# Kernel tuning notes

Measured on AMD Instinct MI355X. Metric: run time of the kernel, lower is better.

The kernel has to match this reference:

```python
import jax, jax.numpy as jnp
import numpy as np

N_NODES = 50000
N_EDGES = 1200000
N_REL = 40
N_BASES = 30
EMB = 64
HID = 128
N_GRAPHS = 64


def rgcn_layer(h, src, dst, edge_type, comp, basis, root, bias):
    # W_r = sum_b comp[r,b] * basis[b]  -> [R, in, out]
    W = jnp.einsum('rb,bio->rio', comp, basis)
    n = h.shape[0]
    # aggregate source features per (target node, relation): mean aggregation (PyG RGCNConv default)
    seg = dst * N_REL + edge_type                      # [E]
    msgs = h[src]                                      # [E, in]  (gather)
    agg = jax.ops.segment_sum(msgs, seg, num_segments=n * N_REL)
    agg = agg.reshape(n, N_REL, -1)                    # [N, R, in]
    cnt = jax.ops.segment_sum(jnp.ones((src.shape[0],), h.dtype), seg,
                              num_segments=n * N_REL).reshape(n, N_REL, 1)
    agg = agg / jnp.maximum(cnt, 1.0)
    out = jnp.einsum('nri,rio->no', agg, W) + h @ root + bias
    return out


def setup_inputs() -> dict:
    key = jax.random.key(0)
    ks = jax.random.split(key, 12)
    x = jnp.arange(N_NODES, dtype=jnp.int64) if jax.config.jax_enable_x64 else jnp.arange(N_NODES, dtype=jnp.int32)
    edge_index = jax.random.randint(ks[0], (2, N_EDGES), 0, N_NODES)
    edge_type = jax.random.randint(ks[1], (N_EDGES,), 0, N_REL)
    batch = jnp.sort(jax.random.randint(ks[2], (N_NODES,), 0, N_GRAPHS))
    s = 0.05
    node_emb = jax.random.normal(ks[3], (N_NODES, EMB), jnp.float32)
    comp1 = jax.random.normal(ks[4], (N_REL, N_BASES), jnp.float32) * s
    basis1 = jax.random.normal(ks[5], (N_BASES, EMB, HID), jnp.float32) * s
    root1 = jax.random.normal(ks[6], (EMB, HID), jnp.float32) * s
    bias1 = jnp.zeros((HID,), jnp.float32)
    comp2 = jax.random.normal(ks[7], (N_REL, N_BASES), jnp.float32) * s
    basis2 = jax.random.normal(ks[8], (N_BASES, HID, HID), jnp.float32) * s
    root2 = jax.random.normal(ks[9], (HID, HID), jnp.float32) * s
    bias2 = jnp.zeros((HID,), jnp.float32)
    return {"x": x, "edge_index": edge_index, "edge_type": edge_type, "batch": batch,
            "node_emb": node_emb,
            "comp1": comp1, "basis1": basis1, "root1": root1, "bias1": bias1,
            "comp2": comp2, "basis2": basis2, "root2": root2, "bias2": bias2}


def reference(x, edge_index, edge_type, batch, node_emb,
              comp1, basis1, root1, bias1, comp2, basis2, root2, bias2):
    src, dst = edge_index[0], edge_index[1]
    h = node_emb[x]                                              # embedding lookup
    h = jax.nn.relu(rgcn_layer(h, src, dst, edge_type, comp1, basis1, root1, bias1))
    h = jax.nn.relu(rgcn_layer(h, src, dst, edge_type, comp2, basis2, root2, bias2))
    # global mean pool over graphs in batch
    sums = jax.ops.segment_sum(h, batch, num_segments=N_GRAPHS)  # [G, HID]
    cnts = jax.ops.segment_sum(jnp.ones((h.shape[0],), h.dtype), batch,
                               num_segments=N_GRAPHS)[:, None]
    return sums / jnp.maximum(cnts, 1.0)
```

## Files before the change

### kernel.cpp

```cpp
#include <hip/hip_runtime.h>


#define N_NODES 50000
#define N_EDGES 1200000
#define N_REL   40
#define N_BASES 30
#define EMB     64
#define HID     128
#define N_GRAPHS 64

#define NKEYC_MAX 160
#define PERM_CAP  ((size_t)N_EDGES + (size_t)NKEYC_MAX * 256)
#define SP_EPB    1024

typedef float f32x4  __attribute__((ext_vector_type(4)));
typedef short bf16x8 __attribute__((ext_vector_type(8)));

__device__ __forceinline__ unsigned short f2bf(float x) {
    unsigned int u = __float_as_uint(x);
    u = (u + 0x7FFFu + ((u >> 16) & 1u)) >> 16;
    return (unsigned short)u;
}
__device__ __forceinline__ float bflo(unsigned int u) { return __uint_as_float(u << 16); }
__device__ __forceinline__ float bfhi(unsigned int u) { return __uint_as_float(u & 0xffff0000u); }

#define OFF_WF1   ((size_t)0)
#define OFF_WF2   ((size_t)163840)
#define OFF_CNT   ((size_t)491520)
#define OFF_H1    ((size_t)2491520)
#define OFF_H2    ((size_t)8891520)
#define OFF_HB1   ((size_t)15291520)
#define OFF_HB2   ((size_t)16891520)
#define OFF_CNTG  ((size_t)20091520)
#define OFF_POOL  ((size_t)20091584)
#define OFF_PSRC  ((size_t)20099776)
#define OFF_POS   ((size_t)21340736)
#define OFF_PDST  ((size_t)22581696)
#define OFF_HCR   ((size_t)23822656)
#define OFF_CCR   ((size_t)23822816)
#define OFF_POCR  ((size_t)23822976)
#define OFF_HD    ((size_t)23823168)
#define OFF_CD    ((size_t)23873168)
#define OFF_POD   ((size_t)23923168)
#define OFF_RF1   ((size_t)23973184)
#define OFF_RF2   ((size_t)23977280)
#define OFF_PM    ((size_t)23985472)

template <int IN, int KT>
__global__ void k_Wfrag(const float* __restrict__ comp, const float* __restrict__ basis,
                        unsigned short* __restrict__ Wf) {
    const int FR = IN * HID;
    int idx = blockIdx.x * blockDim.x + threadIdx.x;
    if (idx >= N_REL * FR) return;
    int r = idx / FR, F = idx - r * FR;
    int j = F & 7, lane = (F >> 3) & 63, tt = F >> 9;
    int kt = tt % KT, ct = tt / KT;
    int k = kt * 32 + (lane >> 4) * 8 + j;
    int c = ct * 16 + (lane & 15);
    float s = 0.f;
#pragma unroll
    for (int b = 0; b < N_BASES; ++b)
        s += comp[r * N_BASES + b] * basis[((size_t)b * IN + k) * HID + c];
    Wf[idx] = f2bf(s);
}

template <int IN, int KT>
__global__ void k_rootfrag(const float* __restrict__ root, unsigned short* __restrict__ rf) {
    int idx = blockIdx.x * blockDim.x + threadIdx.x;
    if (idx >= IN * HID) return;
    int j = idx & 7, lane = (idx >> 3) & 63, tt = idx >> 9;
    int kt = tt % KT, ct = tt / KT;
    int k = kt * 32 + (lane >> 4) * 8 + j;
    int c = ct * 16 + (lane & 15);
    rf[idx] = f2bf(root[k * HID + c]);
}

__global__ void k_count(const int* __restrict__ dst, const int* __restrict__ etype,
                        float* __restrict__ cnt_t) {
    int e = blockIdx.x * blockDim.x + threadIdx.x;
    if (e >= N_EDGES) return;
    atomicAdd(&cnt_t[(size_t)etype[e] * N_NODES + dst[e]], 1.0f);
}

__global__ void k_deg_inv(float* __restrict__ cnt_t, int* __restrict__ hist) {
    int n = blockIdx.x * blockDim.x + threadIdx.x;
    if (n >= N_NODES) return;
    float s = 0.f;
#pragma unroll 8
    for (int r = 0; r < N_REL; ++r) {
        float c = cnt_t[(size_t)r * N_NODES + n];
        s += c;
        cnt_t[(size_t)r * N_NODES + n] = 1.0f / fmaxf(c, 1.0f);
    }
    hist[n] = (int)(s + 0.5f);
}

__global__ void k_scan_d(const int* __restrict__ hist, int* __restrict__ po) {
    __shared__ int csum[256];
    int t = threadIdx.x;
    const int CH = (N_NODES + 255) / 256;
    int k0 = t * CH, k1 = min(k0 + CH, N_NODES);
    int s = 0;
    for (int k = k0; k < k1; ++k) s += hist[k];
    csum[t] = s;
    __syncthreads();
    if (t == 0) {
        int acc = 0;
        for (int i = 0; i < 256; ++i) { int v = csum[i]; csum[i] = acc; acc += v; }
        po[N_NODES] = acc;
    }
    __syncthreads();
    int base = csum[t];
    for (int k = k0; k < k1; ++k) { po[k] = base; base += hist[k]; }
}

__global__ void k_hist_cr(const int* __restrict__ dst, const int* __restrict__ etype,
                          int* __restrict__ hist, int chn, int nkeyc) {
    __shared__ int lh[NKEYC_MAX];
    int t = threadIdx.x;
    if (t < nkeyc) lh[t] = 0;
    __syncthreads();
    int e = blockIdx.x * blockDim.x + t;
    if (e < N_EDGES) atomicAdd(&lh[(dst[e] / chn) * N_REL + etype[e]], 1);
    __syncthreads();
    if (t < nkeyc && lh[t]) atomicAdd(&hist[t], lh[t]);
}

__global__ void k_scan_cr(const int* __restrict__ hist, int* __restrict__ po, int nkeyc) {
    if (threadIdx.x == 0) {
        int acc = 0;
        for (int k = 0; k < nkeyc; ++k) {
            po[k] = acc;
            acc += ((hist[k] + 255) >> 8) << 8;
        }
        po[nkeyc] = acc;
    }
}

__global__ void k_fill(int* __restrict__ ps_src, int* __restrict__ ps_os,
                       int* __restrict__ ps_dst, int dumprow) {
    for (size_t s = (size_t)blockIdx.x * blockDim.x + threadIdx.x; s < PERM_CAP;
         s += (size_t)gridDim.x * blockDim.x) {
        ps_src[s] = 0;
        ps_os[s] = dumprow;
        ps_dst[s] = 0;
    }
}

__global__ void k_scatter_s(const int* __restrict__ src, const int* __restrict__ dst,
                            const int* __restrict__ etype,
                            const int* __restrict__ po_cr, int* __restrict__ cur_cr,
                            const int* __restrict__ po_d, int* __restrict__ cur_d,
                            int* __restrict__ ps_src, int* __restrict__ ps_os,
                            int* __restrict__ ps_dst, int chn, int nkeyc) {
    __shared__ int lh[NKEYC_MAX], sbase[NKEYC_MAX];
    int t = threadIdx.x;
    if (t < nkeyc) lh[t] = 0;
    __syncthreads();
    int e0 = blockIdx.x * SP_EPB;
    int e_[4], key_[4];
#pragma unroll
    for (int i = 0; i < 4; ++i) {
        int e = e0 + t + i * 256;
        e_[i] = e;
        if (e < N_EDGES) {
            key_[i] = (dst[e] / chn) * N_REL + etype[e];
            atomicAdd(&lh[key_[i]], 1);
        }
    }
    __syncthreads();
    if (t < nkeyc) { if (lh[t]) sbase[t] = atomicAdd(&cur_cr[t], lh[t]); lh[t] = 0; }
    __syncthreads();
#pragma unroll
    for (int i = 0; i < 4; ++i) {
        if (e_[i] < N_EDGES) {
            int e = e_[i], key = key_[i];
            int d = dst[e];
            int p = atomicAdd(&lh[key], 1);
            int slot = po_cr[key] + sbase[key] + p;
            int os_g = po_d[d] + atomicAdd(&cur_d[d], 1);
            int os_l = os_g - po_d[(d / chn) * chn];
            ps_src[slot] = src[e];
            ps_os[slot] = os_l;
            ps_dst[slot] = d;
        }
    }
}

template <int IN, int KT>
__global__ __launch_bounds__(256, 4)
void k_rootgemm(const unsigned short* __restrict__ hb_in,
                const unsigned short* __restrict__ rf,
                const float* __restrict__ bias, float* __restrict__ h) {
    __shared__ unsigned short Wl[8 * KT * 64 * 8];
    {
        const f32x4* Wg = (const f32x4*)rf;
        f32x4* Wd = (f32x4*)Wl;
        for (int kk = threadIdx.x; kk < 8 * KT * 64; kk += 256) Wd[kk] = Wg[kk];
    }
    __syncthreads();

    int l = threadIdx.x & 63, wv = threadIdx.x >> 6;
    int lrow = l & 15, lk = l >> 4;
    int nbase = blockIdx.x * 64 + wv * 16;

    int nrow = min(nbase + lrow, N_NODES - 1);
    bf16x8 a[KT];
    const unsigned short* hrow = hb_in + (size_t)nrow * IN + lk * 8;
#pragma unroll
    for (int kt = 0; kt < KT; ++kt)
        a[kt] = *(const bf16x8*)(hrow + kt * 32);

    f32x4 acc[8];
#pragma unroll
    for (int ct = 0; ct < 8; ++ct) acc[ct] = (f32x4){0.f, 0.f, 0.f, 0.f};
#pragma unroll
    for (int ct = 0; ct < 8; ++ct) {
#pragma unroll
        for (int kt = 0; kt < KT; ++kt) {
            bf16x8 bb = *(const bf16x8*)(Wl + ((ct * KT + kt) * 64 + l) * 8);
            acc[ct] = __builtin_amdgcn_mfma_f32_16x16x32_bf16(a[kt], bb, acc[ct], 0, 0, 0);
        }
    }
#pragma unroll
    for (int q = 0; q < 4; ++q) {
        int n = nbase + lk * 4 + q;
        if (n < N_NODES) {
#pragma unroll
            for (int ct = 0; ct < 8; ++ct)
                h[(size_t)n * HID + ct * 16 + lrow] = acc[ct][q] + bias[ct * 16 + lrow];
        }
    }
}

template <int IN, int KT>
__global__ __launch_bounds__(256, 4)
void k_msg(const unsigned short* __restrict__ hb_in, const int* __restrict__ ps_src,
           const int* __restrict__ ps_os, const int* __restrict__ ps_dst,
           const float* __restrict__ invc_t,
           const int* __restrict__ po_cr,
           const unsigned short* __restrict__ Wf, unsigned int* __restrict__ pm) {
    __shared__ unsigned short Wl[8 * KT * 64 * 8];
    int slot0 = po_cr[0] + blockIdx.x * 256;
    if (slot0 >= po_cr[N_REL]) return;
    int r = 0;
    while (po_cr[r + 1] <= slot0) ++r;

    {
        const f32x4* Wg = (const f32x4*)(Wf + (size_t)r * (8 * KT * 64 * 8));
        f32x4* Wd = (f32x4*)Wl;
        for (int kk = threadIdx.x; kk < 8 * KT * 64; kk += 256) Wd[kk] = Wg[kk];
    }
    __syncthreads();

    int l = threadIdx.x & 63, wv = threadIdx.x >> 6;
    int lrow = l & 15, lk = l >> 4;
    const float* invr = invc_t + (size_t)r * N_NODES;

    for (int t = wv; t < 16; t += 4) {
        int slot = slot0 + t * 16 + lrow;
        int sv = ps_src[slot];
        int os = ps_os[slot];
        int d  = ps_dst[slot];
        float inv = invr[d];

        bf16x8 a[KT];
        const unsigned short* hrow = hb_in + (size_t)sv * IN + lk * 8;
#pragma unroll
        for (int kt = 0; kt < KT; ++kt)
            a[kt] = *(const bf16x8*)(hrow + kt * 32);

        f32x4 acc[8];
#pragma unroll
        for (int ct = 0; ct < 8; ++ct) acc[ct] = (f32x4){0.f, 0.f, 0.f, 0.f};
#pragma unroll
        for (int ct = 0; ct < 8; ++ct) {
#pragma unroll
            for (int kt = 0; kt < KT; ++kt) {
                bf16x8 bb = *(const bf16x8*)(Wl + ((ct * KT + kt) * 64 + l) * 8);
                acc[ct] = __builtin_amdgcn_mfma_f32_16x16x32_bf16(a[kt], bb, acc[ct], 0, 0, 0);
            }
        }
#pragma unroll
        for (int q = 0; q < 4; ++q) {
            int row = lk * 4 + q;
            int osq   = __shfl(os, row);
            float ivq = __shfl(inv, row);
            unsigned int* dp = pm + (size_t)osq * 64 + lrow;
#pragma unroll
            for (int cp = 0; cp < 4; ++cp) {
                unsigned int u = (unsigned int)f2bf(acc[2 * cp][q] * ivq)
                               | ((unsigned int)f2bf(acc[2 * cp + 1][q] * ivq) << 16);
                __builtin_nontemporal_store(u, dp + cp * 16);
            }
        }
    }
}

template <bool WRITE_HB>
__global__ __launch_bounds__(256, 8)
void k_reduce(const unsigned int* __restrict__ pm, const int* __restrict__ po_d,
              int n0chunk, int chn, float* __restrict__ h,
              unsigned short* __restrict__ hb_out) {
    int wv = threadIdx.x >> 6, p = threadIdx.x & 63;
    int n = n0chunk + blockIdx.x * 4 + wv;
    if (n >= n0chunk + chn) return;
    int pmbase = po_d[n0chunk];
    int b0 = po_d[n] - pmbase;
    int cn = po_d[n + 1] - pmbase - b0;
    float lo = 0.f, hi = 0.f;
    const unsigned int* rp = pm + (size_t)b0 * 64 + p;
    int k = 0;
    for (; k + 4 <= cn; k += 4) {
        unsigned int u0 = __builtin_nontemporal_load(rp);
        unsigned int u1 = __builtin_nontemporal_load(rp + 64);
        unsigned int u2 = __builtin_nontemporal_load(rp + 128);
        unsigned int u3 = __builtin_nontemporal_load(rp + 192);
        rp += 256;
        lo += bflo(u0) + bflo(u1) + bflo(u2) + bflo(u3);
        hi += bfhi(u0) + bfhi(u1) + bfhi(u2) + bfhi(u3);
    }
    for (; k < cn; ++k) {
        unsigned int u = __builtin_nontemporal_load(rp);
        rp += 64;
        lo += bflo(u); hi += bfhi(u);
    }
    int cA = (p & 15) + 32 * (p >> 4);
    float* hp = h + (size_t)n * HID;
    float vA = fmaxf(hp[cA] + lo, 0.f);
    float vB = fmaxf(hp[cA + 16] + hi, 0.f);
    hp[cA] = vA;
    hp[cA + 16] = vB;
    if (WRITE_HB) {
        hb_out[(size_t)n * HID + cA] = f2bf(vA);
        hb_out[(size_t)n * HID + cA + 16] = f2bf(vB);
    }
}

__global__ void k_cvt_emb(const float* __restrict__ emb, const int* __restrict__ x,
                          unsigned short* __restrict__ hb) {
    int idx = blockIdx.x * blockDim.x + threadIdx.x;
    if (idx >= N_NODES * (EMB / 4)) return;
    int n = idx / (EMB / 4), c4 = idx % (EMB / 4);
    int row = x[n];
    float4 v = *(const float4*)(emb + (size_t)row * EMB + c4 * 4);
    ushort4 o = {f2bf(v.x), f2bf(v.y), f2bf(v.z), f2bf(v.w)};
    *(ushort4*)(hb + (size_t)n * EMB + c4 * 4) = o;
}

__global__ void k_gcount2(const int* __restrict__ batch, float* __restrict__ cntG) {
    int g = threadIdx.x;
    if (g >= N_GRAPHS) return;
    int lo = 0, hi = N_NODES;
    while (lo < hi) { int m = (lo + hi) >> 1; if (batch[m] < g) lo = m + 1; else hi = m; }
    int lb0 = lo;
    lo = 0; hi = N_NODES;
    while (lo < hi) { int m = (lo + hi) >> 1; if (batch[m] < g + 1) lo = m + 1; else hi = m; }
    cntG[g] = (float)(lo - lb0);
}

__global__ void k_pool(const float* __restrict__ h, const int* __restrict__ batch,
                       float* __restrict__ acc) {
    const int CH = 64;
    int n0 = blockIdx.x * CH;
    int o = threadIdx.x;
    int nend = min(n0 + CH, N_NODES);
    if (n0 >= N_NODES) return;
    int curg = batch[n0];
    float run = 0.f;
    for (int n = n0; n < nend; ++n) {
        int g = batch[n];
        if (g != curg) {
            atomicAdd(&acc[(size_t)curg * HID + o], run);
            run = 0.f;
            curg = g;
        }
        run += h[(size_t)n * HID + o];
    }
    atomicAdd(&acc[(size_t)curg * HID + o], run);
}

__global__ void k_final(const float* __restrict__ acc, const float* __restrict__ cntG,
                        float* __restrict__ out) {
    int idx = blockIdx.x * blockDim.x + threadIdx.x;
    if (idx >= N_GRAPHS * HID) return;
    int g = idx >> 7;
    out[idx] = acc[idx] / fmaxf(cntG[g], 1.0f);
}

extern "C" void kernel_launch(void* const* d_in, const int* in_sizes, int n_in,
                              void* d_out, int out_size, void* d_ws, size_t ws_size,
                              hipStream_t stream) {
    const int*   x         = (const int*)d_in[0];
    const int*   edge_index= (const int*)d_in[1];
    const int*   etype     = (const int*)d_in[2];
    const int*   batch     = (const int*)d_in[3];
    const float* node_emb  = (const float*)d_in[4];
    const float* comp1     = (const float*)d_in[5];
    const float* basis1    = (const float*)d_in[6];
    const float* root1     = (const float*)d_in[7];
    const float* bias1     = (const float*)d_in[8];
    const float* comp2     = (const float*)d_in[9];
    const float* basis2    = (const float*)d_in[10];
    const float* root2     = (const float*)d_in[11];
    const float* bias2     = (const float*)d_in[12];
    float* out = (float*)d_out;

    const int* src = edge_index;
    const int* dst = edge_index + N_EDGES;

    float* ws = (float*)d_ws;
    unsigned short* Wf1 = (unsigned short*)(ws + OFF_WF1);
    unsigned short* Wf2 = (unsigned short*)(ws + OFF_WF2);
    float* cnt_t = ws + OFF_CNT;
    float* h1   = ws + OFF_H1;
    float* h2   = ws + OFF_H2;
    unsigned short* hb1 = (unsigned short*)(ws + OFF_HB1);
    unsigned short* hb2 = (unsigned short*)(ws + OFF_HB2);
    float* cntG = ws + OFF_CNTG;
    float* pool = ws + OFF_POOL;
    int*   ps_src = (int*)(ws + OFF_PSRC);
    int*   ps_os  = (int*)(ws + OFF_POS);
    int*   ps_dst = (int*)(ws + OFF_PDST);
    int*   hist_cr = (int*)(ws + OFF_HCR);
    int*   cur_cr  = (int*)(ws + OFF_CCR);
    int*   po_cr   = (int*)(ws + OFF_POCR);
    int*   hist_d  = (int*)(ws + OFF_HD);
    int*   cur_d   = (int*)(ws + OFF_CD);
    int*   po_d    = (int*)(ws + OFF_POD);
    unsigned short* rf1 = (unsigned short*)(ws + OFF_RF1);
    unsigned short* rf2 = (unsigned short*)(ws + OFF_RF2);
    unsigned int* pm = (unsigned int*)(ws + OFF_PM);

    size_t ws_floats = ws_size / sizeof(float);
    int nch = 4;
    if (ws_floats >= OFF_PM + ((size_t)N_EDGES / 1 + 12504) * 64) nch = 1;
    else if (ws_floats >= OFF_PM + ((size_t)N_EDGES / 2 + 12504) * 64) nch = 2;
    int chn = N_NODES / nch;
    int nkeyc = nch * N_REL;
    int capr = N_EDGES / nch + 12504;
    int gridm = (capr + 255) / 256 + N_REL;

    hipMemsetAsync(cnt_t, 0, (size_t)N_NODES * N_REL * sizeof(float), stream);
    hipMemsetAsync(cntG, 0, (size_t)(N_GRAPHS + N_GRAPHS * HID) * sizeof(float), stream);
    hipMemsetAsync(hist_cr, 0, 2 * NKEYC_MAX * sizeof(int), stream);
    hipMemsetAsync(cur_d, 0, N_NODES * sizeof(int), stream);

    k_count<<<(N_EDGES + 255) / 256, 256, 0, stream>>>(dst, etype, cnt_t);
    k_deg_inv<<<(N_NODES + 255) / 256, 256, 0, stream>>>(cnt_t, hist_d);
    k_scan_d<<<1, 256, 0, stream>>>(hist_d, po_d);
    k_hist_cr<<<(N_EDGES + 255) / 256, 256, 0, stream>>>(dst, etype, hist_cr, chn, nkeyc);
    k_scan_cr<<<1, 64, 0, stream>>>(hist_cr, po_cr, nkeyc);
    k_fill<<<2048, 256, 0, stream>>>(ps_src, ps_os, ps_dst, capr - 1);
    k_scatter_s<<<(N_EDGES + SP_EPB - 1) / SP_EPB, 256, 0, stream>>>(
        src, dst, etype, po_cr, cur_cr, po_d, cur_d, ps_src, ps_os, ps_dst, chn, nkeyc);

    k_Wfrag<EMB, 2><<<(N_REL * EMB * HID + 255) / 256, 256, 0, stream>>>(comp1, basis1, Wf1);
    k_Wfrag<HID, 4><<<(N_REL * HID * HID + 255) / 256, 256, 0, stream>>>(comp2, basis2, Wf2);
    k_rootfrag<EMB, 2><<<(EMB * HID + 255) / 256, 256, 0, stream>>>(root1, rf1);
    k_rootfrag<HID, 4><<<(HID * HID + 255) / 256, 256, 0, stream>>>(root2, rf2);

    k_cvt_emb<<<(N_NODES * (EMB / 4) + 255) / 256, 256, 0, stream>>>(node_emb, x, hb1);
    k_rootgemm<EMB, 2><<<(N_NODES + 63) / 64, 256, 0, stream>>>(hb1, rf1, bias1, h1);
    for (int c = 0; c < nch; ++c) {
        k_msg<EMB, 2><<<gridm, 256, 0, stream>>>(hb1, ps_src, ps_os, ps_dst, cnt_t,
                                                 po_cr + c * N_REL, Wf1, pm);
        k_reduce<true><<<chn / 4, 256, 0, stream>>>(pm, po_d, c * chn, chn, h1, hb2);
    }

    k_rootgemm<HID, 4><<<(N_NODES + 63) / 64, 256, 0, stream>>>(hb2, rf2, bias2, h2);
    for (int c = 0; c < nch; ++c) {
        k_msg<HID, 4><<<gridm, 256, 0, stream>>>(hb2, ps_src, ps_os, ps_dst, cnt_t,
                                                 po_cr + c * N_REL, Wf2, pm);
        k_reduce<false><<<chn / 4, 256, 0, stream>>>(pm, po_d, c * chn, chn, h2, nullptr);
    }

    k_gcount2<<<1, 64, 0, stream>>>(batch, cntG);
    k_pool<<<(N_NODES + 63) / 64, HID, 0, stream>>>(h2, batch, pool);
    k_final<<<(N_GRAPHS * HID + 255) / 256, 256, 0, stream>>>(pool, cntG, out);
}
```

Measured before the change: 1.021 ms.

## Fuse count and chunk histogram, fill only pad slots, precompute block relation table

Merges the per-edge count atomics and the chunk/relation histogram into one pass over the edge list, removing a kernel launch and a reread of dst/etype. The full-buffer fill of the permutation arrays is replaced by a per-key kernel that writes only the padding slots at the end of each bucket. A byte table mapping each 256-slot block to its relation is built once, so k_msg looks up its relation directly instead of walking the prefix array. This adds two small launches and relies on the scatter covering every non-pad slot.

```diff
diff --git a/kernel.cpp b/kernel.cpp
--- a/kernel.cpp
+++ b/kernel.cpp
@@ -44,7 +44,8 @@
 #define OFF_POD   ((size_t)23923168)
 #define OFF_RF1   ((size_t)23973184)
 #define OFF_RF2   ((size_t)23977280)
-#define OFF_PM    ((size_t)23985472)
+#define OFF_BREL  ((size_t)23985472)
+#define OFF_PM    ((size_t)23987520)
 
 template <int IN, int KT>
 __global__ void k_Wfrag(const float* __restrict__ comp, const float* __restrict__ basis,
@@ -75,11 +76,21 @@
     rf[idx] = f2bf(root[k * HID + c]);
 }
 
-__global__ void k_count(const int* __restrict__ dst, const int* __restrict__ etype,
-                        float* __restrict__ cnt_t) {
-    int e = blockIdx.x * blockDim.x + threadIdx.x;
-    if (e >= N_EDGES) return;
-    atomicAdd(&cnt_t[(size_t)etype[e] * N_NODES + dst[e]], 1.0f);
+__global__ void k_count_hist(const int* __restrict__ dst, const int* __restrict__ etype,
+                             float* __restrict__ cnt_t, int* __restrict__ hist,
+                             int chn, int nkeyc) {
+    __shared__ int lh[NKEYC_MAX];
+    int t = threadIdx.x;
+    if (t < nkeyc) lh[t] = 0;
+    __syncthreads();
+    int e = blockIdx.x * blockDim.x + t;
+    if (e < N_EDGES) {
+        int d = dst[e], r = etype[e];
+        atomicAdd(&cnt_t[(size_t)r * N_NODES + d], 1.0f);
+        atomicAdd(&lh[(d / chn) * N_REL + r], 1);
+    }
+    __syncthreads();
+    if (t < nkeyc && lh[t]) atomicAdd(&hist[t], lh[t]);
 }
 
 __global__ void k_deg_inv(float* __restrict__ cnt_t, int* __restrict__ hist) {
@@ -114,18 +125,6 @@
     for (int k = k0; k < k1; ++k) { po[k] = base; base += hist[k]; }
 }
 
-__global__ void k_hist_cr(const int* __restrict__ dst, const int* __restrict__ etype,
-                          int* __restrict__ hist, int chn, int nkeyc) {
-    __shared__ int lh[NKEYC_MAX];
-    int t = threadIdx.x;
-    if (t < nkeyc) lh[t] = 0;
-    __syncthreads();
-    int e = blockIdx.x * blockDim.x + t;
-    if (e < N_EDGES) atomicAdd(&lh[(dst[e] / chn) * N_REL + etype[e]], 1);
-    __syncthreads();
-    if (t < nkeyc && lh[t]) atomicAdd(&hist[t], lh[t]);
-}
-
 __global__ void k_scan_cr(const int* __restrict__ hist, int* __restrict__ po, int nkeyc) {
     if (threadIdx.x == 0) {
         int acc = 0;
@@ -137,10 +136,21 @@
     }
 }
 
-__global__ void k_fill(int* __restrict__ ps_src, int* __restrict__ ps_os,
-                       int* __restrict__ ps_dst, int dumprow) {
-    for (size_t s = (size_t)blockIdx.x * blockDim.x + threadIdx.x; s < PERM_CAP;
-         s += (size_t)gridDim.x * blockDim.x) {
+__global__ void k_brel(const int* __restrict__ po, unsigned char* __restrict__ brel,
+                       int nkeyc) {
+    int k = blockIdx.x * blockDim.x + threadIdx.x;
+    if (k >= nkeyc) return;
+    unsigned char r = (unsigned char)(k % N_REL);
+    for (int b = po[k] >> 8; b < (po[k + 1] >> 8); ++b) brel[b] = r;
+}
+
+__global__ void k_fillpads(const int* __restrict__ hist, const int* __restrict__ po,
+                           int* __restrict__ ps_src, int* __restrict__ ps_os,
+                           int* __restrict__ ps_dst, int dumprow, int nkeyc) {
+    int k = blockIdx.x;
+    if (k >= nkeyc) return;
+    int start = po[k] + hist[k], end = po[k + 1];
+    for (int s = start + threadIdx.x; s < end; s += blockDim.x) {
         ps_src[s] = 0;
         ps_os[s] = dumprow;
         ps_dst[s] = 0;
@@ -238,13 +248,13 @@
 void k_msg(const unsigned short* __restrict__ hb_in, const int* __restrict__ ps_src,
            const int* __restrict__ ps_os, const int* __restrict__ ps_dst,
            const float* __restrict__ invc_t,
-           const int* __restrict__ po_cr,
+           const int* __restrict__ po_c,
+           const unsigned char* __restrict__ brel,
            const unsigned short* __restrict__ Wf, unsigned int* __restrict__ pm) {
     __shared__ unsigned short Wl[8 * KT * 64 * 8];
-    int slot0 = po_cr[0] + blockIdx.x * 256;
-    if (slot0 >= po_cr[N_REL]) return;
-    int r = 0;
-    while (po_cr[r + 1] <= slot0) ++r;
+    int slot0 = po_c[0] + blockIdx.x * 256;
+    if (slot0 >= po_c[N_REL]) return;
+    int r = brel[slot0 >> 8];
 
     {
         const f32x4* Wg = (const f32x4*)(Wf + (size_t)r * (8 * KT * 64 * 8));
@@ -430,6 +440,7 @@
     int*   po_d    = (int*)(ws + OFF_POD);
     unsigned short* rf1 = (unsigned short*)(ws + OFF_RF1);
     unsigned short* rf2 = (unsigned short*)(ws + OFF_RF2);
+    unsigned char* brel = (unsigned char*)(ws + OFF_BREL);
     unsigned int* pm = (unsigned int*)(ws + OFF_PM);
 
     size_t ws_floats = ws_size / sizeof(float);
@@ -446,12 +457,14 @@
     hipMemsetAsync(hist_cr, 0, 2 * NKEYC_MAX * sizeof(int), stream);
     hipMemsetAsync(cur_d, 0, N_NODES * sizeof(int), stream);
 
-    k_count<<<(N_EDGES + 255) / 256, 256, 0, stream>>>(dst, etype, cnt_t);
+    k_count_hist<<<(N_EDGES + 255) / 256, 256, 0, stream>>>(dst, etype, cnt_t, hist_cr,
+                                                            chn, nkeyc);
     k_deg_inv<<<(N_NODES + 255) / 256, 256, 0, stream>>>(cnt_t, hist_d);
     k_scan_d<<<1, 256, 0, stream>>>(hist_d, po_d);
-    k_hist_cr<<<(N_EDGES + 255) / 256, 256, 0, stream>>>(dst, etype, hist_cr, chn, nkeyc);
     k_scan_cr<<<1, 64, 0, stream>>>(hist_cr, po_cr, nkeyc);
-    k_fill<<<2048, 256, 0, stream>>>(ps_src, ps_os, ps_dst, capr - 1);
+    k_brel<<<1, 256, 0, stream>>>(po_cr, brel, nkeyc);
+    k_fillpads<<<nkeyc, 256, 0, stream>>>(hist_cr, po_cr, ps_src, ps_os, ps_dst,
+                                          capr - 1, nkeyc);
     k_scatter_s<<<(N_EDGES + SP_EPB - 1) / SP_EPB, 256, 0, stream>>>(
         src, dst, etype, po_cr, cur_cr, po_d, cur_d, ps_src, ps_os, ps_dst, chn, nkeyc);
 
@@ -464,14 +477,14 @@
     k_rootgemm<EMB, 2><<<(N_NODES + 63) / 64, 256, 0, stream>>>(hb1, rf1, bias1, h1);
     for (int c = 0; c < nch; ++c) {
         k_msg<EMB, 2><<<gridm, 256, 0, stream>>>(hb1, ps_src, ps_os, ps_dst, cnt_t,
-                                                 po_cr + c * N_REL, Wf1, pm);
+                                                 po_cr + c * N_REL, brel, Wf1, pm);
         k_reduce<true><<<chn / 4, 256, 0, stream>>>(pm, po_d, c * chn, chn, h1, hb2);
     }
 
     k_rootgemm<HID, 4><<<(N_NODES + 63) / 64, 256, 0, stream>>>(hb2, rf2, bias2, h2);
     for (int c = 0; c < nch; ++c) {
         k_msg<HID, 4><<<gridm, 256, 0, stream>>>(hb2, ps_src, ps_os, ps_dst, cnt_t,
-                                                 po_cr + c * N_REL, Wf2, pm);
+                                                 po_cr + c * N_REL, brel, Wf2, pm);
         k_reduce<false><<<chn / 4, 256, 0, stream>>>(pm, po_d, c * chn, chn, h2, nullptr);
     }
 
```

New measurement: 1.016 ms. No clear change (-0.5%).
